# Optimization experiments

Hardware: AMD Instinct MI355X
Metric: run time of the kernel (lower is better)

The kernel has to match this reference:

```python
import jax, jax.numpy as jnp
import numpy as np

B = 4096                      # flattened tokens
IN_MODES = (16, 16, 16)       # auto_shape(4096, d=3)
OUT_MODES = (16, 16, 16)
RANK = 8                      # tt ranks: (1, 8, 8, 1)


def setup_inputs() -> dict:
    key = jax.random.key(0)
    ks = jax.random.split(key, 4)
    ranks = (1, RANK, RANK, 1)
    x = jax.random.normal(ks[0], (B, int(np.prod(IN_MODES))), dtype=jnp.float32)
    cores = []
    for i in range(3):
        shp = (ranks[i], IN_MODES[i], OUT_MODES[i], ranks[i + 1])
        # glorot-style variance for TT cores (t3.glorot_initializer analogue)
        std = float(np.sqrt(2.0 / (ranks[i] * IN_MODES[i] + OUT_MODES[i] * ranks[i + 1])))
        cores.append(jax.random.normal(ks[i + 1], shp, dtype=jnp.float32) * std)
    bias = 0.001 * jnp.ones((int(np.prod(OUT_MODES)),), dtype=jnp.float32)
    return {"x": x, "core0": cores[0], "core1": cores[1], "core2": cores[2], "bias": bias}


def _tt_matmul(x, core0, core1, core2):
    # dense_tt_matmul: y = x @ W, W the TT-matrix with cores (r_{k-1}, m_k, n_k, r_k)
    Bn = x.shape[0]
    data = x.reshape((Bn,) + IN_MODES)                     # [B, m1, m2, m3]
    # core0 has leading rank 1 -> squeeze it
    res = jnp.einsum('bmxy,mnr->bxynr', data, core0[0])    # [B, m2, m3, n1, r1]
    res = jnp.einsum('bmynr,rmfs->bynfs', res, core1)      # [B, m3, n1, n2, r2]
    res = jnp.einsum('bmnpe,emf->bnpf', res, core2[..., 0])  # [B, n1, n2, n3]
    return res.reshape(Bn, -1)                             # [B, n1*n2*n3]


def reference(x, core0, core1, core2, bias):
    return _tt_matmul(x, core0, core1, core2) + bias
```

## Files before the change

### kernel.cpp

```cpp
#include <hip/hip_runtime.h>


typedef __attribute__((ext_vector_type(8))) short bf16x8;
typedef __attribute__((ext_vector_type(4))) float f32x4;

__device__ __forceinline__ unsigned short f2bf(float f) {
    unsigned u = __builtin_bit_cast(unsigned, f);
    u += 0x7FFFu + ((u >> 16) & 1u);
    return (unsigned short)(u >> 16);
}

__device__ __forceinline__ unsigned f2bf_pk(float lo, float hi) {
#if __has_builtin(__builtin_amdgcn_cvt_pk_bf16_f32)
    typedef __attribute__((ext_vector_type(2))) __bf16 bf2;
    bf2 r = __builtin_amdgcn_cvt_pk_bf16_f32(lo, hi);
    return __builtin_bit_cast(unsigned, r);
#else
    return (unsigned)f2bf(lo) | ((unsigned)f2bf(hi) << 16);
#endif
}

union BF8 { bf16x8 v; unsigned short s[8]; unsigned u[4]; };
union U2 { uint2 d; unsigned u[2]; };

#define S2 136
#define S3 2208
#define R1 40
#define R2 672

__global__ __launch_bounds__(512, 4) void tt_mfma3_v2(
    const float* __restrict__ x, const float* __restrict__ c0,
    const float* __restrict__ c1, const float* __restrict__ c2,
    const float* __restrict__ bias, float* __restrict__ out)
{
    __shared__ __align__(16) unsigned short sT1[4 * S3];
    __shared__ __align__(16) unsigned short sT2[16 * R2];

    const int tid  = threadIdx.x;
    const int w    = tid >> 6;
    const int lane = tid & 63;
    const int q    = lane >> 4;
    const int c    = lane & 15;
    const int qh   = q >> 1, ql = q & 1;

    const int ct1  = w & 3;
    const int rtg1 = w >> 2;
    const int rp2  = w & 3;
    const int vp2  = w >> 2;

    BF8 a0[4];
    #pragma unroll
    for (int i = 0; i < 4; ++i) {
        if (q < 2) {
            const int n1 = (rtg1 * 4 + i) * 2 + (c >> 3), r1 = c & 7;
            const float* p = &c0[(q * 8) * 128 + n1 * 8 + r1];
            #pragma unroll
            for (int u = 0; u < 4; ++u)
                a0[i].u[u] = f2bf_pk(p[(2 * u) * 128], p[(2 * u + 1) * 128]);
        } else {
            a0[i].u[0] = a0[i].u[1] = a0[i].u[2] = a0[i].u[3] = 0;
        }
    }
    BF8 aF[2][4];
    #pragma unroll
    for (int i = 0; i < 2; ++i) {
        const int n2 = (rp2 * 2 + i) * 2 + (c >> 3), r2 = c & 7;
        #pragma unroll
        for (int k4 = 0; k4 < 4; ++k4) {
            const float* p = &c1[(k4 * 4 + q) * 128 + n2 * 8 + r2];
            #pragma unroll
            for (int u = 0; u < 4; ++u)
                aF[i][k4].u[u] = f2bf_pk(p[(2 * u) * 2048], p[(2 * u + 1) * 2048]);
        }
    }
    BF8 a2[4];
    #pragma unroll
    for (int s = 0; s < 4; ++s) {
        const float* p = &c2[(s * 4 + q) * 16 + c];
        #pragma unroll
        for (int u = 0; u < 4; ++u)
            a2[s].u[u] = f2bf_pk(p[(2 * u) * 256], p[(2 * u + 1) * 256]);
    }

    unsigned short* const w1p = &sT1[(c >> 2) * S3 + (ct1 * 4 + (c & 3)) * S2
                                     + (rtg1 * 8 + qh) * 8 + 4 * ql];
    const int xoff = q * 2048 + (ct1 * 4 + (c & 3)) * 16 + (c >> 2);
    const unsigned short* const r2p = &sT1[(vp2 * 2) * S3 + q * S2 + c * 8];
    unsigned short* const w2p = &sT2[(rp2 * 4 + qh) * R2 + c * R1
                                     + vp2 * 16 + 4 * ql];
    const unsigned short* const r3p = &sT2[(w * 2) * R2 + c * R1 + q * 8];

    const f32x4 zero = {0.f, 0.f, 0.f, 0.f};

    for (int tok = 0; tok < 4; ++tok) {
        const int b = blockIdx.x * 4 + tok;
        const float* xb = x + (size_t)b * 4096;

        f32x4 acc3[2] = {zero, zero};

        auto G1 = [&](int s) {
            BF8 bx;
            if (q < 2) {
                const float* xp = xb + xoff + s * 4;
                #pragma unroll
                for (int u = 0; u < 4; ++u)
                    bx.u[u] = f2bf_pk(xp[(2 * u) * 256], xp[(2 * u + 1) * 256]);
            } else {
                bx.u[0] = bx.u[1] = bx.u[2] = bx.u[3] = 0;
            }
            #pragma unroll
            for (int i = 0; i < 4; ++i) {
                f32x4 d = __builtin_amdgcn_mfma_f32_16x16x32_bf16(a0[i].v, bx.v, zero, 0, 0, 0);
                U2 t; t.u[0] = f2bf_pk(d[0], d[1]); t.u[1] = f2bf_pk(d[2], d[3]);
                *(uint2*)(w1p + i * 16) = t.d;
            }
        };

        G1(0);
        #pragma unroll
        for (int s = 0; s < 4; ++s) {
            __syncthreads();
            f32x4 acc2[2][2] = {{zero, zero}, {zero, zero}};
            #pragma unroll
            for (int k4 = 0; k4 < 4; ++k4) {
                bf16x8 b0 = *(const bf16x8*)(r2p + k4 * 544);
                bf16x8 b1 = *(const bf16x8*)(r2p + S3 + k4 * 544);
                #pragma unroll
                for (int i = 0; i < 2; ++i) {
                    acc2[i][0] = __builtin_amdgcn_mfma_f32_16x16x32_bf16(aF[i][k4].v, b0, acc2[i][0], 0, 0, 0);
                    acc2[i][1] = __builtin_amdgcn_mfma_f32_16x16x32_bf16(aF[i][k4].v, b1, acc2[i][1], 0, 0, 0);
                }
            }
            #pragma unroll
            for (int i = 0; i < 2; ++i) {
                #pragma unroll
                for (int j = 0; j < 2; ++j) {
                    U2 t;
                    t.u[0] = f2bf_pk(acc2[i][j][0], acc2[i][j][1]);
                    t.u[1] = f2bf_pk(acc2[i][j][2], acc2[i][j][3]);
                    *(uint2*)(w2p + i * 1344 + j * 8) = t.d;
                }
            }
            __syncthreads();
            {
                bf16x8 b0 = *(const bf16x8*)(r3p);
                bf16x8 b1 = *(const bf16x8*)(r3p + R2);
                acc3[0] = __builtin_amdgcn_mfma_f32_16x16x32_bf16(a2[s].v, b0, acc3[0], 0, 0, 0);
                acc3[1] = __builtin_amdgcn_mfma_f32_16x16x32_bf16(a2[s].v, b1, acc3[1], 0, 0, 0);
            }
            if (s < 3) G1(s + 1);
        }

        float* outb = out + (size_t)b * 4096;
        #pragma unroll
        for (int t = 0; t < 2; ++t) {
            const int idx = c * 256 + (w * 2 + t) * 16 + 4 * q;
            f32x4 bv = *(const f32x4*)&bias[idx];
            f32x4 o = acc3[t] + bv;
            *(f32x4*)&outb[idx] = o;
        }
    }
}

extern "C" void kernel_launch(void* const* d_in, const int* in_sizes, int n_in,
                              void* d_out, int out_size, void* d_ws, size_t ws_size,
                              hipStream_t stream) {
    const float* x    = (const float*)d_in[0];
    const float* c0   = (const float*)d_in[1];
    const float* c1   = (const float*)d_in[2];
    const float* c2   = (const float*)d_in[3];
    const float* bias = (const float*)d_in[4];
    float* out = (float*)d_out;

    tt_mfma3_v2<<<1024, 512, 0, stream>>>(x, c0, c1, c2, bias, out);
}
```

Before: 174.4 us.

## Prefetch next token's x with vector loads and process eight tokens per block

Each token's x slice is now loaded with 16-byte vector loads into registers and packed to bf16 ahead of time. The next token's load is issued during the last stage of the current token, so global latency overlaps with MFMA work. Blocks now handle eight tokens instead of four, halving the grid and amortising the per-block conversion of the core weights. The x column mapping is permuted, with the core2 indexing adjusted to match, and s_setprio is raised around the MFMA loop. In exchange it uses more registers and has fewer blocks, which may reduce occupancy and load balance.

```diff
diff --git a/kernel.cpp b/kernel.cpp
--- a/kernel.cpp
+++ b/kernel.cpp
@@ -21,14 +21,16 @@
 }
 
 union BF8 { bf16x8 v; unsigned short s[8]; unsigned u[4]; };
-union U2 { uint2 d; unsigned u[2]; };
+union U2  { uint2 d; unsigned u[2]; };
 
 #define S2 136
 #define S3 2208
 #define R1 40
 #define R2 672
 
-__global__ __launch_bounds__(512, 4) void tt_mfma3_v2(
+#define MFMA32 __builtin_amdgcn_mfma_f32_16x16x32_bf16
+
+__global__ __launch_bounds__(512, 4) void tt_mfma3_v5(
     const float* __restrict__ x, const float* __restrict__ c0,
     const float* __restrict__ c1, const float* __restrict__ c2,
     const float* __restrict__ bias, float* __restrict__ out)
@@ -47,6 +49,39 @@
     const int rtg1 = w >> 2;
     const int rp2  = w & 3;
     const int vp2  = w >> 2;
+
+    unsigned short* const w1p = &sT1[(c >> 2) * S3 + (ct1 * 4 + (c & 3)) * S2
+                                     + (rtg1 * 8 + qh) * 8 + 4 * ql];
+    const unsigned short* const r2p = &sT1[(vp2 * 2) * S3 + q * S2 + c * 8];
+    unsigned short* const w2p = &sT2[(rp2 * 4 + qh) * R2 + c * R1
+                                     + vp2 * 16 + 4 * ql];
+    const unsigned short* const r3p = &sT2[(w * 2) * R2 + c * R1 + q * 8];
+    const int xcol = ct1 * 64 + (c & 3) * 16 + (c >> 2) * 4;
+
+    const f32x4 zero = {0.f, 0.f, 0.f, 0.f};
+
+    BF8 xpk[4];
+    #pragma unroll
+    for (int s = 0; s < 4; ++s)
+        xpk[s].u[0] = xpk[s].u[1] = xpk[s].u[2] = xpk[s].u[3] = 0;
+
+    auto issue_x = [&](int tb) {
+        if (q < 2) {
+            const float* xb = x + (size_t)(blockIdx.x * 8 + tb) * 4096;
+            f32x4 t[8];
+            #pragma unroll
+            for (int j = 0; j < 8; ++j)
+                t[j] = *(const f32x4*)&xb[(q * 8 + j) * 256 + xcol];
+            #pragma unroll
+            for (int s = 0; s < 4; ++s) {
+                #pragma unroll
+                for (int u = 0; u < 4; ++u)
+                    xpk[s].u[u] = f2bf_pk(t[2 * u][s], t[2 * u + 1][s]);
+            }
+        }
+    };
+
+    issue_x(0);
 
     BF8 a0[4];
     #pragma unroll
@@ -76,61 +111,44 @@
     BF8 a2[4];
     #pragma unroll
     for (int s = 0; s < 4; ++s) {
-        const float* p = &c2[(s * 4 + q) * 16 + c];
+        const float* p = &c2[(q * 4 + s) * 16 + c];
         #pragma unroll
         for (int u = 0; u < 4; ++u)
             a2[s].u[u] = f2bf_pk(p[(2 * u) * 256], p[(2 * u + 1) * 256]);
     }
 
-    unsigned short* const w1p = &sT1[(c >> 2) * S3 + (ct1 * 4 + (c & 3)) * S2
-                                     + (rtg1 * 8 + qh) * 8 + 4 * ql];
-    const int xoff = q * 2048 + (ct1 * 4 + (c & 3)) * 16 + (c >> 2);
-    const unsigned short* const r2p = &sT1[(vp2 * 2) * S3 + q * S2 + c * 8];
-    unsigned short* const w2p = &sT2[(rp2 * 4 + qh) * R2 + c * R1
-                                     + vp2 * 16 + 4 * ql];
-    const unsigned short* const r3p = &sT2[(w * 2) * R2 + c * R1 + q * 8];
+    auto G1 = [&](int s2) {
+        #pragma unroll
+        for (int i = 0; i < 4; ++i) {
+            f32x4 d = MFMA32(a0[i].v, xpk[s2].v, zero, 0, 0, 0);
+            U2 t; t.u[0] = f2bf_pk(d[0], d[1]); t.u[1] = f2bf_pk(d[2], d[3]);
+            *(uint2*)(w1p + i * 16) = t.d;
+        }
+    };
 
-    const f32x4 zero = {0.f, 0.f, 0.f, 0.f};
-
-    for (int tok = 0; tok < 4; ++tok) {
-        const int b = blockIdx.x * 4 + tok;
-        const float* xb = x + (size_t)b * 4096;
+    for (int tok = 0; tok < 8; ++tok) {
+        const int b = blockIdx.x * 8 + tok;
 
         f32x4 acc3[2] = {zero, zero};
-
-        auto G1 = [&](int s) {
-            BF8 bx;
-            if (q < 2) {
-                const float* xp = xb + xoff + s * 4;
-                #pragma unroll
-                for (int u = 0; u < 4; ++u)
-                    bx.u[u] = f2bf_pk(xp[(2 * u) * 256], xp[(2 * u + 1) * 256]);
-            } else {
-                bx.u[0] = bx.u[1] = bx.u[2] = bx.u[3] = 0;
-            }
-            #pragma unroll
-            for (int i = 0; i < 4; ++i) {
-                f32x4 d = __builtin_amdgcn_mfma_f32_16x16x32_bf16(a0[i].v, bx.v, zero, 0, 0, 0);
-                U2 t; t.u[0] = f2bf_pk(d[0], d[1]); t.u[1] = f2bf_pk(d[2], d[3]);
-                *(uint2*)(w1p + i * 16) = t.d;
-            }
-        };
 
         G1(0);
         #pragma unroll
         for (int s = 0; s < 4; ++s) {
             __syncthreads();
+            if (s == 3 && tok < 7) issue_x(tok + 1);
             f32x4 acc2[2][2] = {{zero, zero}, {zero, zero}};
+            __builtin_amdgcn_s_setprio(1);
             #pragma unroll
             for (int k4 = 0; k4 < 4; ++k4) {
                 bf16x8 b0 = *(const bf16x8*)(r2p + k4 * 544);
                 bf16x8 b1 = *(const bf16x8*)(r2p + S3 + k4 * 544);
                 #pragma unroll
                 for (int i = 0; i < 2; ++i) {
-                    acc2[i][0] = __builtin_amdgcn_mfma_f32_16x16x32_bf16(aF[i][k4].v, b0, acc2[i][0], 0, 0, 0);
-                    acc2[i][1] = __builtin_amdgcn_mfma_f32_16x16x32_bf16(aF[i][k4].v, b1, acc2[i][1], 0, 0, 0);
+                    acc2[i][0] = MFMA32(aF[i][k4].v, b0, acc2[i][0], 0, 0, 0);
+                    acc2[i][1] = MFMA32(aF[i][k4].v, b1, acc2[i][1], 0, 0, 0);
                 }
             }
+            __builtin_amdgcn_s_setprio(0);
             #pragma unroll
             for (int i = 0; i < 2; ++i) {
                 #pragma unroll
@@ -145,8 +163,8 @@
             {
                 bf16x8 b0 = *(const bf16x8*)(r3p);
                 bf16x8 b1 = *(const bf16x8*)(r3p + R2);
-                acc3[0] = __builtin_amdgcn_mfma_f32_16x16x32_bf16(a2[s].v, b0, acc3[0], 0, 0, 0);
-                acc3[1] = __builtin_amdgcn_mfma_f32_16x16x32_bf16(a2[s].v, b1, acc3[1], 0, 0, 0);
+                acc3[0] = MFMA32(a2[s].v, b0, acc3[0], 0, 0, 0);
+                acc3[1] = MFMA32(a2[s].v, b1, acc3[1], 0, 0, 0);
             }
             if (s < 3) G1(s + 1);
         }
@@ -172,5 +190,5 @@
     const float* bias = (const float*)d_in[4];
     float* out = (float*)d_out;
 
-    tt_mfma3_v2<<<1024, 512, 0, stream>>>(x, c0, c1, c2, bias, out);
+    tt_mfma3_v5<<<512, 512, 0, stream>>>(x, c0, c1, c2, bias, out);
 }
```

After: 171.3 us. About the same (-1.8%).
